# Kernel optimization log

Hardware: AMD Instinct MI355X
Metric: run time of the kernel (lower is better)

Reference implementation:

```python
import math
import jax, jax.numpy as jnp
import numpy as np

V, D, A, H, FF, L, MD = 500, 512, 512, 8, 2048, 6, 512
HD = A // H
B, S, T = 32, 512, 128


def setup_inputs() -> dict:
    key = jax.random.key(0)
    ks = jax.random.split(key, 40)
    init = lambda k, shape: (jax.random.normal(k, shape, jnp.float32) * 0.02)
    inp = {
        'memory': jax.random.normal(ks[0], (B, S, MD), jnp.float32),
        'memory_lens': jax.random.randint(ks[1], (B,), S // 2, S + 1),
        'ys_in_pad': jax.random.randint(ks[2], (B, T), 0, V),
        'ys_in_lens': jax.random.randint(ks[3], (B,), T // 2, T + 1),
        'emb': init(ks[4], (V, D)),
        'w_out': init(ks[5], (D, V)),
        'b_out': jnp.zeros((V,), jnp.float32),
        # per-layer params stacked on leading L axis (consumed by lax.scan)
        'ln_sa_g': jnp.ones((L, D), jnp.float32), 'ln_sa_b': jnp.zeros((L, D), jnp.float32),
        'sa_wq': init(ks[6], (L, D, A)), 'sa_bq': init(ks[7], (L, A)),
        'sa_wk': init(ks[8], (L, D, A)), 'sa_bk': init(ks[9], (L, A)),
        'sa_wv': init(ks[10], (L, D, A)), 'sa_bv': init(ks[11], (L, A)),
        'sa_wo': init(ks[12], (L, A, D)), 'sa_bo': init(ks[13], (L, D)),
        'ln_ca_g': jnp.ones((L, D), jnp.float32), 'ln_ca_b': jnp.zeros((L, D), jnp.float32),
        'ca_wq': init(ks[14], (L, D, A)), 'ca_bq': init(ks[15], (L, A)),
        'ca_wk': init(ks[16], (L, MD, A)), 'ca_bk': init(ks[17], (L, A)),
        'ca_wv': init(ks[18], (L, MD, A)), 'ca_bv': init(ks[19], (L, A)),
        'ca_wo': init(ks[20], (L, A, D)), 'ca_bo': init(ks[21], (L, D)),
        'ln_ff_g': jnp.ones((L, D), jnp.float32), 'ln_ff_b': jnp.zeros((L, D), jnp.float32),
        'ff_w1': init(ks[22], (L, D, FF)), 'ff_b1': init(ks[23], (L, FF)),
        'ff_w2': init(ks[24], (L, FF, D)), 'ff_b2': init(ks[25], (L, D)),
    }
    return inp


def _layernorm(x, g, b, eps=1e-5):
    m = jnp.mean(x, axis=-1, keepdims=True)
    v = jnp.mean(jnp.square(x - m), axis=-1, keepdims=True)
    return (x - m) * jax.lax.rsqrt(v + eps) * g + b


def _mha(q_in, k_in, v_in, mask, wq, bq, wk, bk, wv, bv, wo, bo):
    # mask: True = disallowed. (B, T, S) for self-attn, (B, 1, S) for cross-attn.
    b_, tq, _ = q_in.shape
    ts = k_in.shape[1]
    q = (q_in @ wq + bq).reshape(b_, tq, H, HD).transpose(0, 2, 1, 3)
    k = (k_in @ wk + bk).reshape(b_, ts, H, HD).transpose(0, 2, 1, 3)
    v = (v_in @ wv + bv).reshape(b_, ts, H, HD).transpose(0, 2, 1, 3)
    s = jnp.einsum('bhtd,bhsd->bhts', q, k) / math.sqrt(HD)
    # penalize_abs_values_gt(limit=50, penalty=1e-4) is identity in the forward
    # pass (it only injects an auxiliary gradient during training).
    s = jnp.where(mask[:, None, :, :], -jnp.inf, s)
    a = jax.nn.softmax(s, axis=-1)  # dropout p=0.0 in this config
    o = jnp.einsum('bhts,bhsd->bhtd', a, v).transpose(0, 2, 1, 3).reshape(b_, tq, A)
    return o @ wo + bo


def _forward(memory, memory_lens, ys_in_pad, ys_in_lens, emb, w_out, b_out, layer_params):
    t = ys_in_pad.shape[1]
    # make_pad_mask | ~subsequent_mask  -> (B, T, T), True = masked
    pad = jnp.arange(t)[None, :] >= ys_in_lens[:, None]            # (B, T)
    causal = ~jnp.tril(jnp.ones((t, t), bool))                     # (T, T)
    tgt_mask = pad[:, None, :] | causal[None]                      # (B, T, T)
    mem_mask = (jnp.arange(memory.shape[1])[None, :] >= memory_lens[:, None])[:, None, :]

    # embedding + sinusoidal positional encoding (dropout in eval = identity)
    pos = jnp.arange(t, dtype=jnp.float32)[:, None]
    div = jnp.exp(jnp.arange(0, D, 2, dtype=jnp.float32) * (-math.log(10000.0) / D))
    pe = jnp.zeros((t, D), jnp.float32)
    pe = pe.at[:, 0::2].set(jnp.sin(pos * div)).at[:, 1::2].set(jnp.cos(pos * div))
    x = emb[ys_in_pad] * math.sqrt(D) + pe[None]

    def step(tgt, p):
        tn = _layernorm(tgt, p['ln_sa_g'], p['ln_sa_b'])
        tgt = tgt + _mha(tn, tn, tn, tgt_mask,
                         p['sa_wq'], p['sa_bq'], p['sa_wk'], p['sa_bk'],
                         p['sa_wv'], p['sa_bv'], p['sa_wo'], p['sa_bo'])
        tn = _layernorm(tgt, p['ln_ca_g'], p['ln_ca_b'])
        tgt = tgt + _mha(tn, memory, memory, mem_mask,
                         p['ca_wq'], p['ca_bq'], p['ca_wk'], p['ca_bk'],
                         p['ca_wv'], p['ca_bv'], p['ca_wo'], p['ca_bo'])
        tn = _layernorm(tgt, p['ln_ff_g'], p['ln_ff_b'])
        h = tn @ p['ff_w1'] + p['ff_b1']
        h = h * jax.nn.sigmoid(h)  # Swish
        tgt = tgt + h @ p['ff_w2'] + p['ff_b2']
        return tgt, None

    x, _ = jax.lax.scan(step, x, layer_params)
    return x @ w_out + b_out  # (B, T, V) logits


_LAYER_KEYS = ['ln_sa_g', 'ln_sa_b', 'sa_wq', 'sa_bq', 'sa_wk', 'sa_bk', 'sa_wv', 'sa_bv',
               'sa_wo', 'sa_bo', 'ln_ca_g', 'ln_ca_b', 'ca_wq', 'ca_bq', 'ca_wk', 'ca_bk',
               'ca_wv', 'ca_bv', 'ca_wo', 'ca_bo', 'ln_ff_g', 'ln_ff_b',
               'ff_w1', 'ff_b1', 'ff_w2', 'ff_b2']


def reference(memory, memory_lens, ys_in_pad, ys_in_lens, emb, w_out, b_out,
              ln_sa_g, ln_sa_b, sa_wq, sa_bq, sa_wk, sa_bk, sa_wv, sa_bv, sa_wo, sa_bo,
              ln_ca_g, ln_ca_b, ca_wq, ca_bq, ca_wk, ca_bk, ca_wv, ca_bv, ca_wo, ca_bo,
              ln_ff_g, ln_ff_b, ff_w1, ff_b1, ff_w2, ff_b2):
    loc = locals()
    layer_params = {k: loc[k] for k in _LAYER_KEYS}
    return _forward(memory, memory_lens, ys_in_pad, ys_in_lens, emb, w_out, b_out, layer_params)
```

## Files before the change

kernel.cpp:

```cpp
#include <hip/hip_runtime.h>
#include <hip/hip_bf16.h>
#include <hip/hip_fp16.h>

constexpr int Bc = 32, Sc = 512, Tc = 128, Dc = 512, Ac = 512, Hc = 8;
constexpr int HDc = 64, FFc = 2048, Lc = 6, Vc = 500;
constexpr int NTOK = Bc * Tc;
constexpr int NMEM = Bc * Sc;

typedef unsigned short u16;
typedef __attribute__((ext_vector_type(8))) short short8;
typedef __attribute__((ext_vector_type(4))) float f32x4;

__device__ __forceinline__ u16 bfc(float x) {
  __hip_bfloat16 h = __float2bfloat16(x);
  return *reinterpret_cast<u16*>(&h);
}

__device__ __forceinline__ void gload16(const void* g, void* l) {
  __builtin_amdgcn_global_load_lds(
      (const __attribute__((address_space(1))) unsigned int*)g,
      (__attribute__((address_space(3))) unsigned int*)l, 16, 0, 0);
}

__device__ __forceinline__ float wave_sum(float v) {
#pragma unroll
  for (int o = 32; o > 0; o >>= 1) v += __shfl_down(v, o);
  return v;
}
__device__ __forceinline__ float wave_max(float v) {
#pragma unroll
  for (int o = 32; o > 0; o >>= 1) v = fmaxf(v, __shfl_down(v, o));
  return v;
}

__global__ __launch_bounds__(256) void embed_pe_k(const int* __restrict__ ys,
                                                  const float* __restrict__ emb,
                                                  float* __restrict__ x) {
  int tok = blockIdx.x;
  int t = tok & (Tc - 1);
  int id = ys[tok];
  int j = threadIdx.x;
  int d0 = 2 * j;
  const float cdiv = -9.210340371976184f / (float)Dc;
  float div = expf((float)d0 * cdiv);
  float ang = (float)t * div;
  float pe0 = sinf(ang), pe1 = cosf(ang);
  const float sc = 22.627416997969522f;
  long base = (long)tok * Dc + d0;
  long ebase = (long)id * Dc + d0;
  x[base]     = emb[ebase]     * sc + pe0;
  x[base + 1] = emb[ebase + 1] * sc + pe1;
}

__global__ __launch_bounds__(256) void layernorm_k(const float* __restrict__ x,
                                                   const float* __restrict__ g,
                                                   const float* __restrict__ bta,
                                                   u16* __restrict__ out) {
  int row = blockIdx.x;
  int tid = threadIdx.x;
  const float* xr = x + (long)row * Dc;
  float2 xv = *(const float2*)(xr + tid * 2);
  __shared__ float red[4];
  float s = wave_sum(xv.x + xv.y);
  if ((tid & 63) == 0) red[tid >> 6] = s;
  __syncthreads();
  float mean = (red[0] + red[1] + red[2] + red[3]) * (1.0f / Dc);
  float dx0 = xv.x - mean, dx1 = xv.y - mean;
  __syncthreads();
  float s2 = wave_sum(dx0 * dx0 + dx1 * dx1);
  if ((tid & 63) == 0) red[tid >> 6] = s2;
  __syncthreads();
  float var = (red[0] + red[1] + red[2] + red[3]) * (1.0f / Dc);
  float rstd = rsqrtf(var + 1e-5f);
  ushort2 o;
  o.x = bfc(dx0 * rstd * g[2 * tid] + bta[2 * tid]);
  o.y = bfc(dx1 * rstd * g[2 * tid + 1] + bta[2 * tid + 1]);
  *(ushort2*)(out + (long)row * Dc + tid * 2) = o;
}

__global__ __launch_bounds__(256) void wtrans_k(const float* __restrict__ src,
                                                u16* __restrict__ dst,
                                                int K, int N, long srcStride, long dstStride) {
  int z = blockIdx.z;
  src += z * srcStride;
  dst += z * dstStride;
  __shared__ float t[32][33];
  int n0 = blockIdx.x * 32, k0 = blockIdx.y * 32;
  int tx = threadIdx.x & 31, ty = threadIdx.x >> 5;
#pragma unroll
  for (int i = 0; i < 4; i++) {
    int n = n0 + tx;
    t[ty + 8 * i][tx] = (n < N) ? src[(long)(k0 + ty + 8 * i) * N + n] : 0.0f;
  }
  __syncthreads();
#pragma unroll
  for (int i = 0; i < 4; i++) {
    dst[(long)(n0 + ty + 8 * i) * K + k0 + tx] = bfc(t[tx][ty + 8 * i]);
  }
}

struct PtrPack8 { const float* p[8]; };
__global__ __launch_bounds__(256) void wtrans8_k(PtrPack8 P, u16* __restrict__ Wt,
                                                 long PLW) {
  int z = blockIdx.z;
  int widx = z / 6, l = z - widx * 6;
  const float* src = P.p[widx] + (long)l * 262144;
  u16* dst = Wt + (long)widx * 262144 + (long)l * PLW;
  __shared__ float t[32][33];
  int n0 = blockIdx.x * 32, k0 = blockIdx.y * 32;
  int tx = threadIdx.x & 31, ty = threadIdx.x >> 5;
#pragma unroll
  for (int i = 0; i < 4; i++)
    t[ty + 8 * i][tx] = src[(long)(k0 + ty + 8 * i) * 512 + n0 + tx];
  __syncthreads();
#pragma unroll
  for (int i = 0; i < 4; i++)
    dst[(long)(n0 + ty + 8 * i) * 512 + k0 + tx] = bfc(t[tx][ty + 8 * i]);
}

__global__ __launch_bounds__(256) void f2b_k(const float* __restrict__ in,
                                             u16* __restrict__ out, long n) {
  long i = ((long)blockIdx.x * 256 + threadIdx.x) * 4;
  if (i >= n) return;
  float4 v = *(const float4*)(in + i);
  ushort4 o;
  o.x = bfc(v.x); o.y = bfc(v.y); o.z = bfc(v.z); o.w = bfc(v.w);
  *(ushort4*)(out + i) = o;
}

template <int BMW, int OMODE, bool BIAS, bool RES, bool SWISH, bool NCH, bool MLEN>
__global__ __launch_bounds__(256) void mgemm_k(
    const u16* __restrict__ A, const u16* __restrict__ Bt,
    const float* __restrict__ bias0, const float* __restrict__ bias1,
    const float* __restrict__ bias2,
    void* __restrict__ Cv, const float* __restrict__ R, const int* __restrict__ mlens,
    int N, int K, int lda, int ldb, int ldc, int nbi,
    long batAo, long batAi, long batBo, long batBi, long batCo, long batCi) {
  constexpr int BM = BMW * 32;

  int gx = gridDim.x, gy = gridDim.y;
  int nwg = gx * gy * gridDim.z;
  int orig = blockIdx.x + gx * (blockIdx.y + gy * blockIdx.z);
  int q = nwg >> 3, r = nwg & 7, xcd = orig & 7, off = orig >> 3;
  int wgid = (xcd < r ? xcd * (q + 1) : r * (q + 1) + (xcd - r) * q) + off;
  int bxi = wgid % gx; int tmp = wgid / gx;
  int byi = tmp % gy;  int bzi = tmp / gy;

  int z = bzi;
  int bo = z / nbi, bi = z - bo * nbi;
  int m0 = byi * BM, n0 = bxi * 128;

  if constexpr (MLEN) {
    if ((m0 & 511) >= mlens[m0 >> 9]) return;
  }

  const u16* Ab = A + bo * batAo + bi * batAi;
  const u16* Bb = Bt + bo * batBo + bi * batBi;
  long coff = bo * batCo + bi * batCi;
  const float* bias = nullptr;
  if constexpr (BIAS) bias = (bi == 0) ? bias0 : ((bi == 1) ? bias1 : bias2);

  __shared__ __align__(16) u16 As[2][BM * 32];
  __shared__ __align__(16) u16 Bs[2][128 * 32];

  int tid = threadIdx.x;
  int lane = tid & 63, wid = tid >> 6;
  int wm = wid >> 1, wn = wid & 1;
  int fr = lane & 15, grp = lane >> 4;

  f32x4 acc[BMW][4];
#pragma unroll
  for (int i = 0; i < BMW; i++)
#pragma unroll
    for (int j = 0; j < 4; j++) acc[i][j] = (f32x4){0.f, 0.f, 0.f, 0.f};

  const u16* ga = Ab + (long)(m0 + (tid >> 2)) * lda + ((tid & 3) << 3);
  const u16* gb = Bb + (long)(n0 + (tid >> 2)) * ldb + ((tid & 3) << 3);

  auto STAGE = [&](int buf, int kt) {
    u16* lA = &As[buf][tid * 8];
    u16* lB = &Bs[buf][tid * 8];
    gload16(ga + kt, lA);
    if constexpr (BM == 128) gload16(ga + kt + (long)64 * lda, lA + 2048);
    gload16(gb + kt, lB);
    gload16(gb + kt + (long)64 * ldb, lB + 2048);
  };

  auto COMPUTE = [&](int buf) {
    short8 av[BMW], bv[4];
#pragma unroll
    for (int i = 0; i < BMW; i++)
      av[i] = *(const short8*)&As[buf][(wm * BMW * 16 + i * 16 + fr) * 32 + grp * 8];
#pragma unroll
    for (int j = 0; j < 4; j++)
      bv[j] = *(const short8*)&Bs[buf][(wn * 64 + j * 16 + fr) * 32 + grp * 8];
#pragma unroll
    for (int i = 0; i < BMW; i++)
#pragma unroll
      for (int j = 0; j < 4; j++)
        acc[i][j] = __builtin_amdgcn_mfma_f32_16x16x32_bf16(av[i], bv[j], acc[i][j], 0, 0, 0);
  };

  STAGE(0, 0);
  __syncthreads();
  int cur = 0;
  for (int kt = 32; kt < K; kt += 32) {
    STAGE(cur ^ 1, kt);
    COMPUTE(cur);
    __syncthreads();
    cur ^= 1;
  }
  COMPUTE(cur);

  int rbase = m0 + wm * BMW * 16 + grp * 4;
  int cbase = n0 + wn * 64 + fr;
#pragma unroll
  for (int i = 0; i < BMW; i++) {
#pragma unroll
    for (int j = 0; j < 4; j++) {
      int col = cbase + j * 16;
      if (NCH && col >= N) continue;
      float bb = 0.0f;
      if constexpr (BIAS) bb = bias[col];
#pragma unroll
      for (int r2 = 0; r2 < 4; r2++) {
        int row = rbase + i * 16 + r2;
        float v = acc[i][j][r2] + bb;
        long idx = coff + (long)row * ldc + col;
        if constexpr (RES) v += R[idx];
        if constexpr (SWISH) v = v / (1.0f + expf(-v));
        if constexpr (OMODE == 0) ((u16*)Cv)[idx] = bfc(v);
        else ((float*)Cv)[idx] = v;
      }
    }
  }
}

template <int SKV, int KVBLK, bool CAUSAL, int IQ>
__global__ __launch_bounds__(256) void fattn_k(
    const u16* __restrict__ Q, const u16* __restrict__ Kg, const u16* __restrict__ Vg,
    u16* __restrict__ O, const int* __restrict__ lens) {
  constexpr int NJ  = KVBLK / 16;
  constexpr int NKV = KVBLK / 32;
  constexpr int NT  = SKV / KVBLK;
  constexpr int KST = 72;
  constexpr int VST = KVBLK + 8;
  constexpr int WR  = 16 * IQ;
  constexpr int WGR = 64 * IQ;
  constexpr int CH  = KVBLK / 32;

  __shared__ __align__(16) u16 Ks[KVBLK * KST];
  __shared__ __align__(16) u16 Vs[64 * VST];
  __shared__ __align__(16) u16 Ps[WGR * VST];

  int bh = blockIdx.x; int b = bh >> 3, h = bh & 7;
  int row00 = blockIdx.y * WGR;
  int tid = threadIdx.x, lane = tid & 63, wid = tid >> 6;
  int fr = lane & 15, grp = lane >> 4;
  int len = lens[b];
  int row0w = row00 + wid * WR;

  short8 qa[IQ][2];
  {
    const u16* qp = Q + ((long)b * Tc + row0w + fr) * 512 + h * 64 + grp * 8;
#pragma unroll
    for (int i = 0; i < IQ; i++)
#pragma unroll
      for (int k2 = 0; k2 < 2; k2++)
        qa[i][k2] = *(const short8*)(qp + (long)i * 16 * 512 + k2 * 32);
  }

  float m_run[IQ][4], l_run[IQ][4];
  f32x4 acc_o[IQ][4];
#pragma unroll
  for (int i = 0; i < IQ; i++)
#pragma unroll
    for (int r = 0; r < 4; r++) { m_run[i][r] = -1e30f; l_run[i][r] = 0.0f; }
#pragma unroll
  for (int i = 0; i < IQ; i++)
#pragma unroll
    for (int j = 0; j < 4; j++) acc_o[i][j] = (f32x4){0.f, 0.f, 0.f, 0.f};

  const u16* Kbase = Kg + ((long)b * SKV) * 512 + h * 64;
  const u16* Vbase = Vg + ((long)b * SKV) * 512 + h * 64;

  int NTeff = NT;
  if constexpr (CAUSAL) NTeff = (row00 + WGR - 1) / KVBLK + 1;
  int lenT = (len + KVBLK - 1) / KVBLK;
  if (lenT < NTeff) NTeff = lenT;

  short8 kreg[CH], vreg[CH];
#pragma unroll
  for (int c = 0; c < CH; c++) {
    int idx = tid + 256 * c; int kv = idx >> 3, s = idx & 7;
    kreg[c] = *(const short8*)(Kbase + (long)kv * 512 + s * 8);
    vreg[c] = *(const short8*)(Vbase + (long)kv * 512 + s * 8);
  }

  for (int t = 0; t < NTeff; t++) {
    int kv0 = t * KVBLK;
    __syncthreads();
#pragma unroll
    for (int c = 0; c < CH; c++) {
      int idx = tid + 256 * c; int kv = idx >> 3, s = idx & 7;
      *(short8*)&Ks[kv * KST + s * 8] = kreg[c];
#pragma unroll
      for (int j = 0; j < 8; j++)
        Vs[(s * 8 + j) * VST + kv] = (u16)vreg[c][j];
    }
    __syncthreads();
    if (t + 1 < NTeff) {
      int kvn = kv0 + KVBLK;
#pragma unroll
      for (int c = 0; c < CH; c++) {
        int idx = tid + 256 * c; int kv = idx >> 3, s = idx & 7;
        kreg[c] = *(const short8*)(Kbase + (long)(kvn + kv) * 512 + s * 8);
        vreg[c] = *(const short8*)(Vbase + (long)(kvn + kv) * 512 + s * 8);
      }
    }

    int jmax = NJ;
    if constexpr (CAUSAL) {
      jmax = (row0w + WR - 1 - kv0) / 16 + 1;
      if (jmax > NJ) jmax = NJ;
    }

    f32x4 accs[IQ][NJ];
    __builtin_amdgcn_s_setprio(1);
#pragma unroll
    for (int j = 0; j < NJ; j++) {
      if (CAUSAL && j >= jmax) continue;
      short8 bv0 = *(const short8*)&Ks[(j * 16 + fr) * KST + grp * 8];
      short8 bv1 = *(const short8*)&Ks[(j * 16 + fr) * KST + 32 + grp * 8];
#pragma unroll
      for (int i = 0; i < IQ; i++) {
        f32x4 a = __builtin_amdgcn_mfma_f32_16x16x32_bf16(qa[i][0], bv0, (f32x4){0.f,0.f,0.f,0.f}, 0, 0, 0);
        accs[i][j] = __builtin_amdgcn_mfma_f32_16x16x32_bf16(qa[i][1], bv1, a, 0, 0, 0);
      }
    }
    __builtin_amdgcn_s_setprio(0);

    float alpha[IQ][4];
#pragma unroll
    for (int i = 0; i < IQ; i++) {
#pragma unroll
      for (int r = 0; r < 4; r++) {
        int qrow = row0w + i * 16 + grp * 4 + r;
        float vmax = -1e30f;
#pragma unroll
        for (int j = 0; j < NJ; j++) {
          if (CAUSAL && j >= jmax) continue;
          int kvb = kv0 + j * 16 + fr;
          float s = accs[i][j][r] * 0.125f;
          bool msk = (kvb >= len) || (CAUSAL && kvb > qrow);
          s = msk ? -1e30f : s;
          accs[i][j][r] = s;
          vmax = fmaxf(vmax, s);
        }
        vmax = fmaxf(vmax, __shfl_xor(vmax, 1));
        vmax = fmaxf(vmax, __shfl_xor(vmax, 2));
        vmax = fmaxf(vmax, __shfl_xor(vmax, 4));
        vmax = fmaxf(vmax, __shfl_xor(vmax, 8));
        float mn = fmaxf(m_run[i][r], vmax);
        float al = __expf(m_run[i][r] - mn);
        m_run[i][r] = mn;
        alpha[i][r] = al;
        float rs = 0.0f;
#pragma unroll
        for (int j = 0; j < NJ; j++) {
          if (CAUSAL && j >= jmax) continue;
          float p = __expf(accs[i][j][r] - mn);
          accs[i][j][r] = p;
          rs += p;
        }
        rs += __shfl_xor(rs, 1);
        rs += __shfl_xor(rs, 2);
        rs += __shfl_xor(rs, 4);
        rs += __shfl_xor(rs, 8);
        l_run[i][r] = l_run[i][r] * al + rs;
      }
    }

#pragma unroll
    for (int i = 0; i < IQ; i++)
#pragma unroll
      for (int j = 0; j < NJ; j++) {
        if (CAUSAL && j >= jmax) continue;
#pragma unroll
        for (int r = 0; r < 4; r++) {
          int prow = wid * WR + i * 16 + grp * 4 + r;
          Ps[prow * VST + j * 16 + fr] = bfc(accs[i][j][r]);
        }
      }

#pragma unroll
    for (int i = 0; i < IQ; i++)
#pragma unroll
      for (int jd = 0; jd < 4; jd++)
#pragma unroll
        for (int r = 0; r < 4; r++)
          acc_o[i][jd][r] *= alpha[i][r];

    int kvmax = NKV;
    if constexpr (CAUSAL) {
      kvmax = (row0w + WR - 1 - kv0) / 32 + 1;
      if (kvmax > NKV) kvmax = NKV;
    }
    __builtin_amdgcn_s_setprio(1);
#pragma unroll
    for (int kk = 0; kk < NKV; kk++) {
      if (CAUSAL && kk >= kvmax) continue;
      short8 pa[IQ];
#pragma unroll
      for (int i = 0; i < IQ; i++)
        pa[i] = *(const short8*)&Ps[(wid * WR + i * 16 + fr) * VST + kk * 32 + grp * 8];
#pragma unroll
      for (int jd = 0; jd < 4; jd++) {
        short8 vb = *(const short8*)&Vs[(jd * 16 + fr) * VST + kk * 32 + grp * 8];
#pragma unroll
        for (int i = 0; i < IQ; i++)
          acc_o[i][jd] = __builtin_amdgcn_mfma_f32_16x16x32_bf16(pa[i], vb, acc_o[i][jd], 0, 0, 0);
      }
    }
    __builtin_amdgcn_s_setprio(0);
  }

#pragma unroll
  for (int i = 0; i < IQ; i++) {
#pragma unroll
    for (int r = 0; r < 4; r++) {
      float inv = 1.0f / l_run[i][r];
      long tok = (long)b * Tc + row0w + i * 16 + grp * 4 + r;
#pragma unroll
      for (int jd = 0; jd < 4; jd++)
        O[tok * 512 + h * 64 + jd * 16 + fr] = bfc(acc_o[i][jd][r] * inv);
    }
  }
}

extern "C" void kernel_launch(void* const* d_in, const int* in_sizes, int n_in,
                              void* d_out, int out_size, void* d_ws, size_t ws_size,
                              hipStream_t stream) {
  const float* memory   = (const float*)d_in[0];
  const int*   mem_lens = (const int*)d_in[1];
  const int*   ys       = (const int*)d_in[2];
  const int*   ys_lens  = (const int*)d_in[3];
  const float* emb      = (const float*)d_in[4];
  const float* w_out    = (const float*)d_in[5];
  const float* b_out    = (const float*)d_in[6];
  const float* pp[26];
  for (int i = 0; i < 26; i++) pp[i] = (const float*)d_in[7 + i];

  constexpr long PLW = 4194304;
  constexpr long OFF_SAQ = 0, OFF_SAK = 262144, OFF_SAV = 524288, OFF_SAO = 786432,
                 OFF_CAQ = 1048576, OFF_CAK = 1310720, OFF_CAV = 1572864,
                 OFF_CAO = 1835008, OFF_FF1 = 2097152, OFF_FF2 = 3145728,
                 OFF_WOUT = 6 * PLW;
  u16*   Wt   = (u16*)d_ws;
  float* X    = (float*)(Wt + 25427968);
  u16*   TO   = (u16*)(X + 2097152);
  u16*   QKV  = TO + 2097152;
  u16*   memb = QKV + 3 * 2097152;
  u16*   Kb   = memb + 8388608;
  u16*   SCR  = Kb + 8388608;
  float* OUT  = (float*)d_out;

  PtrPack8 P8;
  P8.p[0] = pp[2];  P8.p[1] = pp[4];  P8.p[2] = pp[6];  P8.p[3] = pp[8];
  P8.p[4] = pp[12]; P8.p[5] = pp[14]; P8.p[6] = pp[16]; P8.p[7] = pp[18];
  wtrans8_k<<<dim3(16, 16, 48), 256, 0, stream>>>(P8, Wt, PLW);
  wtrans_k<<<dim3(64, 16, Lc), 256, 0, stream>>>(pp[22], Wt + OFF_FF1, 512, 2048, 1048576, PLW);
  wtrans_k<<<dim3(16, 64, Lc), 256, 0, stream>>>(pp[24], Wt + OFF_FF2, 2048, 512, 1048576, PLW);
  wtrans_k<<<dim3(16, 16, 1), 256, 0, stream>>>(w_out, Wt + OFF_WOUT, 512, 500, 0, 0);

  f2b_k<<<(NMEM * Dc / 4 + 255) / 256, 256, 0, stream>>>(memory, memb, (long)NMEM * Dc);
  embed_pe_k<<<NTOK, 256, 0, stream>>>(ys, emb, X);

  for (int l = 0; l < Lc; l++) {
    const u16* WtL = Wt + (long)l * PLW;

    layernorm_k<<<NTOK, 256, 0, stream>>>(X, pp[0] + (long)l * Dc, pp[1] + (long)l * Dc, TO);
    mgemm_k<4, 0, true, false, false, false, false><<<dim3(4, 32, 3), 256, 0, stream>>>(
        TO, WtL + OFF_SAQ, pp[3] + (long)l * Ac, pp[5] + (long)l * Ac, pp[7] + (long)l * Ac,
        QKV, nullptr, nullptr, 512, 512, 512, 512, 512, 3, 0, 0, 0, 262144, 0, 2097152);
    fattn_k<128, 128, true, 2><<<dim3(256, 1), 256, 0, stream>>>(
        QKV, QKV + 2097152, QKV + 2 * 2097152, TO, ys_lens);
    mgemm_k<2, 1, true, true, false, false, false><<<dim3(4, 64, 1), 256, 0, stream>>>(
        TO, WtL + OFF_SAO, pp[9] + (long)l * Dc, nullptr, nullptr, X, X, nullptr,
        512, 512, 512, 512, 512, 1, 0, 0, 0, 0, 0, 0);

    layernorm_k<<<NTOK, 256, 0, stream>>>(X, pp[10] + (long)l * Dc, pp[11] + (long)l * Dc, TO);
    mgemm_k<2, 0, true, false, false, false, false><<<dim3(4, 64, 1), 256, 0, stream>>>(
        TO, WtL + OFF_CAQ, pp[13] + (long)l * Ac, nullptr, nullptr, QKV, nullptr, nullptr,
        512, 512, 512, 512, 512, 1, 0, 0, 0, 0, 0, 0);
    mgemm_k<4, 0, true, false, false, false, true><<<dim3(4, 128, 2), 256, 0, stream>>>(
        memb, WtL + OFF_CAK, pp[15] + (long)l * Ac, pp[17] + (long)l * Ac, nullptr,
        Kb, nullptr, mem_lens, 512, 512, 512, 512, 512, 2, 0, 0, 0, 262144, 0, 8388608);
    fattn_k<512, 128, false, 1><<<dim3(256, 2), 256, 0, stream>>>(
        QKV, Kb, SCR, TO, mem_lens);
    mgemm_k<2, 1, true, true, false, false, false><<<dim3(4, 64, 1), 256, 0, stream>>>(
        TO, WtL + OFF_CAO, pp[19] + (long)l * Dc, nullptr, nullptr, X, X, nullptr,
        512, 512, 512, 512, 512, 1, 0, 0, 0, 0, 0, 0);

    layernorm_k<<<NTOK, 256, 0, stream>>>(X, pp[20] + (long)l * Dc, pp[21] + (long)l * Dc, TO);
    mgemm_k<4, 0, true, false, true, false, false><<<dim3(16, 32, 1), 256, 0, stream>>>(
        TO, WtL + OFF_FF1, pp[23] + (long)l * FFc, nullptr, nullptr, SCR, nullptr, nullptr,
        2048, 512, 512, 512, 2048, 1, 0, 0, 0, 0, 0, 0);
    mgemm_k<2, 1, true, true, false, false, false><<<dim3(4, 64, 1), 256, 0, stream>>>(
        SCR, WtL + OFF_FF2, pp[25] + (long)l * Dc, nullptr, nullptr, X, X, nullptr,
        512, 2048, 2048, 2048, 512, 1, 0, 0, 0, 0, 0, 0);
  }

  f2b_k<<<(NTOK * Dc / 4 + 255) / 256, 256, 0, stream>>>(X, TO, (long)NTOK * Dc);
  mgemm_k<2, 1, true, false, false, true, false><<<dim3(4, 64, 1), 256, 0, stream>>>(
      TO, Wt + OFF_WOUT, b_out, nullptr, nullptr, OUT, nullptr, nullptr,
      500, 512, 512, 512, 500, 1, 0, 0, 0, 0, 0, 0);
}
```

Baseline: 1.225 ms.

## Triple-buffer GEMM K-loop with explicit vmcnt waits; single-pass layernorm stats

The bf16 MFMA GEMM moves from a double-buffered LDS pipeline with __syncthreads to a three-stage ring. Two tiles are kept in flight using global_load_lds, with explicit s_waitcnt vmcnt counts and raw barriers, so load latency overlaps more compute. Layernorm now computes sum and sum of squares in one reduction pass, which removes a barrier round. The cost is 50% more LDS (lower occupancy risk), a dependence on exact vmcnt accounting, and a less numerically stable E[x^2]-mean^2 variance.

```diff
diff --git a/kernel.cpp b/kernel.cpp
--- a/kernel.cpp
+++ b/kernel.cpp
@@ -20,6 +20,26 @@
   __builtin_amdgcn_global_load_lds(
       (const __attribute__((address_space(1))) unsigned int*)g,
       (__attribute__((address_space(3))) unsigned int*)l, 16, 0, 0);
+}
+
+template <int N>
+__device__ __forceinline__ void waitv() {
+  if constexpr (N == 8)      asm volatile("s_waitcnt vmcnt(8)" ::: "memory");
+  else if constexpr (N == 6) asm volatile("s_waitcnt vmcnt(6)" ::: "memory");
+  else if constexpr (N == 4) asm volatile("s_waitcnt vmcnt(4)" ::: "memory");
+  else if constexpr (N == 3) asm volatile("s_waitcnt vmcnt(3)" ::: "memory");
+  else                       asm volatile("s_waitcnt vmcnt(0)" ::: "memory");
+  __builtin_amdgcn_sched_barrier(0);
+}
+__device__ __forceinline__ void barrier_fenced() {
+  __builtin_amdgcn_s_barrier();
+  __builtin_amdgcn_sched_barrier(0);
+}
+__device__ __forceinline__ void lgk0_barrier() {
+  asm volatile("s_waitcnt lgkmcnt(0)" ::: "memory");
+  __builtin_amdgcn_sched_barrier(0);
+  __builtin_amdgcn_s_barrier();
+  __builtin_amdgcn_sched_barrier(0);
 }
 
 __device__ __forceinline__ float wave_sum(float v) {
@@ -60,18 +80,21 @@
   int tid = threadIdx.x;
   const float* xr = x + (long)row * Dc;
   float2 xv = *(const float2*)(xr + tid * 2);
-  __shared__ float red[4];
-  float s = wave_sum(xv.x + xv.y);
-  if ((tid & 63) == 0) red[tid >> 6] = s;
+  float s  = xv.x + xv.y;
+  float s2 = xv.x * xv.x + xv.y * xv.y;
+  __shared__ float red[4], red2[4];
+#pragma unroll
+  for (int o = 32; o > 0; o >>= 1) {
+    s  += __shfl_down(s, o);
+    s2 += __shfl_down(s2, o);
+  }
+  if ((tid & 63) == 0) { red[tid >> 6] = s; red2[tid >> 6] = s2; }
   __syncthreads();
   float mean = (red[0] + red[1] + red[2] + red[3]) * (1.0f / Dc);
+  float ms   = (red2[0] + red2[1] + red2[2] + red2[3]) * (1.0f / Dc);
+  float var  = ms - mean * mean;
+  float rstd = rsqrtf(var + 1e-5f);
   float dx0 = xv.x - mean, dx1 = xv.y - mean;
-  __syncthreads();
-  float s2 = wave_sum(dx0 * dx0 + dx1 * dx1);
-  if ((tid & 63) == 0) red[tid >> 6] = s2;
-  __syncthreads();
-  float var = (red[0] + red[1] + red[2] + red[3]) * (1.0f / Dc);
-  float rstd = rsqrtf(var + 1e-5f);
   ushort2 o;
   o.x = bfc(dx0 * rstd * g[2 * tid] + bta[2 * tid]);
   o.y = bfc(dx1 * rstd * g[2 * tid + 1] + bta[2 * tid + 1]);
@@ -137,6 +160,7 @@
     int N, int K, int lda, int ldb, int ldc, int nbi,
     long batAo, long batAi, long batBo, long batBi, long batCo, long batCi) {
   constexpr int BM = BMW * 32;
+  constexpr int LPS = (BM == 128 ? 2 : 1) + 2;
 
   int gx = gridDim.x, gy = gridDim.y;
   int nwg = gx * gy * gridDim.z;
@@ -160,8 +184,8 @@
   const float* bias = nullptr;
   if constexpr (BIAS) bias = (bi == 0) ? bias0 : ((bi == 1) ? bias1 : bias2);
 
-  __shared__ __align__(16) u16 As[2][BM * 32];
-  __shared__ __align__(16) u16 Bs[2][128 * 32];
+  __shared__ __align__(16) u16 As[3][BM * 32];
+  __shared__ __align__(16) u16 Bs[3][128 * 32];
 
   int tid = threadIdx.x;
   int lane = tid & 63, wid = tid >> 6;
@@ -201,16 +225,21 @@
         acc[i][j] = __builtin_amdgcn_mfma_f32_16x16x32_bf16(av[i], bv[j], acc[i][j], 0, 0, 0);
   };
 
+  int NT = K >> 5;
   STAGE(0, 0);
-  __syncthreads();
-  int cur = 0;
-  for (int kt = 32; kt < K; kt += 32) {
-    STAGE(cur ^ 1, kt);
-    COMPUTE(cur);
-    __syncthreads();
-    cur ^= 1;
-  }
-  COMPUTE(cur);
+  STAGE(1, 32);
+  int cbuf = 0, sbuf = 2, kt = 64;
+  for (int t = 0; t < NT - 2; ++t) {
+    STAGE(sbuf, kt); kt += 32;
+    waitv<2 * LPS>();
+    barrier_fenced();
+    COMPUTE(cbuf);
+    lgk0_barrier();
+    sbuf = cbuf; cbuf = (cbuf == 2) ? 0 : cbuf + 1;
+  }
+  waitv<LPS>();  barrier_fenced(); COMPUTE(cbuf); lgk0_barrier();
+  cbuf = (cbuf == 2) ? 0 : cbuf + 1;
+  waitv<0>();    barrier_fenced(); COMPUTE(cbuf);
 
   int rbase = m0 + wm * BMW * 16 + grp * 4;
   int cbase = n0 + wn * 64 + fr;
```

After: 1.185 ms. -3.2%, faster.
